# Performance work log

Hardware: AMD Instinct MI355X
Metric: run time of the kernel (lower is better)

The kernel has to match this reference:

```python
import jax, jax.numpy as jnp
import numpy as np
from jax import lax

D_MODEL, D_STATE, D_CONV = 64, 16, 4
D_INNER = 2 * D_MODEL          # expand=2 -> 128
DT_RANK = (D_MODEL + 15) // 16 # 4
DIM_IN, LIN_DIM, DIM_OUT = 5881, 128, 256
B, T = 64, 256


def setup_inputs() -> dict:
    key = jax.random.key(0)
    ks = jax.random.split(key, 20)
    s = 0.02
    inp = {
        "input": jax.random.normal(ks[0], (B, T, DIM_IN), dtype=jnp.float32),
        # encoder (SparseLinear dim_in -> 64)
        "W_enc": jax.random.normal(ks[1], (D_MODEL, DIM_IN), dtype=jnp.float32) * s,
        "b_enc": jax.random.normal(ks[2], (D_MODEL,), dtype=jnp.float32) * s,
        # Mamba params
        "W_in": jax.random.normal(ks[3], (2 * D_INNER, D_MODEL), dtype=jnp.float32) * s,
        "conv_w": jax.random.normal(ks[4], (D_INNER, D_CONV), dtype=jnp.float32) * s,
        "conv_b": jax.random.normal(ks[5], (D_INNER,), dtype=jnp.float32) * s,
        "W_x": jax.random.normal(ks[6], (DT_RANK + 2 * D_STATE, D_INNER), dtype=jnp.float32) * s,
        "W_dt": jax.random.normal(ks[7], (D_INNER, DT_RANK), dtype=jnp.float32) * s,
        "b_dt": jax.random.normal(ks[8], (D_INNER,), dtype=jnp.float32) * s,
        "A_log": jnp.log(jnp.broadcast_to(jnp.arange(1, D_STATE + 1, dtype=jnp.float32), (D_INNER, D_STATE))),
        "D_skip": jnp.ones((D_INNER,), dtype=jnp.float32),
        "W_out": jax.random.normal(ks[9], (D_MODEL, D_INNER), dtype=jnp.float32) * s,
        # heads
        "W_fc": jax.random.normal(ks[10], (LIN_DIM, D_MODEL), dtype=jnp.float32) * s,
        "b_fc": jax.random.normal(ks[11], (LIN_DIM,), dtype=jnp.float32) * s,
        "W_mu": jax.random.normal(ks[12], (DIM_OUT, LIN_DIM), dtype=jnp.float32) * s,
        "b_mu": jax.random.normal(ks[13], (DIM_OUT,), dtype=jnp.float32) * s,
        "W_sig": jax.random.normal(ks[14], (DIM_OUT, LIN_DIM), dtype=jnp.float32) * s,
        "b_sig": jax.random.normal(ks[15], (DIM_OUT,), dtype=jnp.float32) * s,
    }
    return inp


def _mamba(z, W_in, conv_w, conv_b, W_x, W_dt, b_dt, A_log, D_skip, W_out):
    # z: [B, T, d_model]
    xz = jnp.einsum("btm,im->bti", z, W_in)            # [B,T,2*Di]
    x, gate = jnp.split(xz, 2, axis=-1)                 # each [B,T,Di]
    # causal depthwise conv1d, kernel D_CONV
    xp = jnp.pad(x, ((0, 0), (D_CONV - 1, 0), (0, 0)))
    x_conv = sum(xp[:, k:k + x.shape[1], :] * conv_w[:, k] for k in range(D_CONV)) + conv_b
    x_conv = jax.nn.silu(x_conv)
    # input-dependent SSM params
    x_dbl = jnp.einsum("btd,id->bti", x_conv, W_x)      # [B,T,dt_rank+2N]
    dt, Bm, Cm = jnp.split(x_dbl, [DT_RANK, DT_RANK + D_STATE], axis=-1)
    dt = jax.nn.softplus(jnp.einsum("btr,dr->btd", dt, W_dt) + b_dt)  # [B,T,Di]
    A = -jnp.exp(A_log)                                 # [Di,N]
    dA = jnp.exp(dt[..., None] * A)                     # [B,T,Di,N]
    dBx = dt[..., None] * Bm[:, :, None, :] * x_conv[..., None]  # [B,T,Di,N]
    # selective scan over time
    def step(h, inp):
        dA_t, dBx_t, C_t = inp
        h = dA_t * h + dBx_t
        y = jnp.einsum("bdn,bn->bd", h, C_t)
        return h, y
    h0 = jnp.zeros((z.shape[0], D_INNER, D_STATE), dtype=z.dtype)
    _, ys = lax.scan(step, h0, (jnp.moveaxis(dA, 1, 0), jnp.moveaxis(dBx, 1, 0), jnp.moveaxis(Cm, 1, 0)))
    y = jnp.moveaxis(ys, 0, 1) + D_skip * x_conv        # [B,T,Di]
    y = y * jax.nn.silu(gate)
    return jnp.einsum("btd,md->btm", y, W_out)          # [B,T,d_model]


def reference(input, W_enc, b_enc, W_in, conv_w, conv_b, W_x, W_dt, b_dt,
              A_log, D_skip, W_out, W_fc, b_fc, W_mu, b_mu, W_sig, b_sig):
    # per-timestep (sparse) linear encoder, vectorized over time
    z = jnp.einsum("btf,df->btd", input, W_enc) + b_enc   # [B,T,64]
    e = _mamba(z, W_in, conv_w, conv_b, W_x, W_dt, b_dt, A_log, D_skip, W_out)
    e = e.mean(axis=1)                                    # [B,64]; dropout = identity (eval)
    x = jax.nn.elu(jnp.tanh(e @ W_fc.T + b_fc))           # [B,128]
    mu = x @ W_mu.T + b_mu                                # [B,256]
    sigma = jax.nn.elu(x @ W_sig.T + b_sig) + 1.0 + 1e-14 # [B,256]
    return (x, mu, sigma)
```

## Files before the change

### kernel.cpp

```cpp
#include <hip/hip_runtime.h>

typedef unsigned short u16;
typedef unsigned int   u32;

#define BB   64
#define TT   256
#define DIN  5881
#define DM   64
#define DI   128
#define NST  16
#define DTR  4
#define TCH  32
#define NCH  8

#define NROW (BB*TT)
#define NKT  92
#define KHALF 46

#define ZWS_OFF  ((size_t)0)
#define WP_OFF   ((size_t)2*1024*1024)
#define PSG_OFF  ((size_t)3*1024*1024)
#define BC_OFF   ((size_t)35*1024*1024)
#define YS_OFF   ((size_t)37*1024*1024)

__device__ __forceinline__ float bf2f(u16 u) {
    union { u32 i; float f; } v; v.i = ((u32)u) << 16; return v.f;
}
__device__ __forceinline__ u16 f2bf(float f) {
    union { float f; u32 i; } v; v.f = f;
    u32 x = v.i;
    return (u16)((x + 0x7FFFu + ((x >> 16) & 1u)) >> 16);
}

typedef __attribute__((ext_vector_type(8))) short short8;
typedef __attribute__((ext_vector_type(4))) float floatx4;

template<bool BF16>
__device__ __forceinline__ float ld1(const void* p, size_t i) {
    if (BF16) return bf2f(((const u16*)p)[i]);
    else      return ((const float*)p)[i];
}
template<bool BF16>
__device__ __forceinline__ u16 ldb(const void* p, size_t i) {
    if (BF16) return ((const u16*)p)[i];
    else      return f2bf(((const float*)p)[i]);
}
template<bool BF16>
__device__ __forceinline__ void st1(void* p, size_t i, float v) {
    if (BF16) ((u16*)p)[i] = f2bf(v);
    else      ((float*)p)[i] = v;
}

__device__ __forceinline__ short8 as_s8(uint4 v) {
    union { uint4 u; short8 s; } c; c.u = v; return c.s;
}

template<bool BF16>
__device__ __forceinline__ void pack_body(const void* Wenc, u16* wp) {
    int g = blockIdx.x * 256 + threadIdx.x;
    if (g >= NKT * 8 * 64) return;
    int lane = g & 63;  int p = g >> 6;
    int kt = p & 1, nt = (p >> 1) & 3, it = p >> 3;
    int r16 = lane & 15, quad = lane >> 4;
    int n  = nt * 16 + r16;
    int k0 = it * 64 + kt * 32 + quad * 8;
    u32 w[4];
    #pragma unroll
    for (int j = 0; j < 4; ++j) {
        int ka = k0 + 2 * j;
        u32 lo = (ka     < DIN) ? (u32)ldb<BF16>(Wenc, (size_t)n * DIN + ka)     : 0u;
        u32 hi = (ka + 1 < DIN) ? (u32)ldb<BF16>(Wenc, (size_t)n * DIN + ka + 1) : 0u;
        w[j] = lo | (hi << 16);
    }
    *(uint4*)(wp + ((size_t)p * 64 + lane) * 8) = make_uint4(w[0], w[1], w[2], w[3]);
}

__global__ __launch_bounds__(256) void pack_wenc(const void* Wenc, const void* A_log, u16* wp) {
    if (((const u32*)A_log)[0] != 0u) pack_body<true >(Wenc, wp);
    else                              pack_body<false>(Wenc, wp);
}

template<bool BF16>
__device__ __forceinline__ void enc_load(const void* inp, const uint4* wp4,
        size_t arow, int it, int kq, int lane, bool tail,
        uint4 a[2], uint4 b[4][2]) {
    #pragma unroll
    for (int kt = 0; kt < 2; ++kt) {
        int k0 = it * 64 + kt * 32 + kq;
        u32 w[4];
        #pragma unroll
        for (int j = 0; j < 4; ++j) {
            u32 lo, hi;
            if (!tail) {
                lo = ldb<BF16>(inp, arow + k0 + 2 * j);
                hi = ldb<BF16>(inp, arow + k0 + 2 * j + 1);
            } else {
                int ka = k0 + 2 * j;
                lo = (ka     < DIN) ? (u32)ldb<BF16>(inp, arow + ka)     : 0u;
                hi = (ka + 1 < DIN) ? (u32)ldb<BF16>(inp, arow + ka + 1) : 0u;
            }
            w[j] = lo | (hi << 16);
        }
        a[kt] = make_uint4(w[0], w[1], w[2], w[3]);
    }
    const uint4* p = wp4 + (size_t)it * 512 + lane;
    #pragma unroll
    for (int nt = 0; nt < 4; ++nt)
        #pragma unroll
        for (int kt = 0; kt < 2; ++kt)
            b[nt][kt] = p[(nt * 2 + kt) * 64];
}

__device__ __forceinline__ void enc_mma(const uint4 a[2], const uint4 b[4][2], floatx4 acc[4]) {
    #pragma unroll
    for (int nt = 0; nt < 4; ++nt)
        #pragma unroll
        for (int kt = 0; kt < 2; ++kt)
            acc[nt] = __builtin_amdgcn_mfma_f32_16x16x32_bf16(
                          as_s8(a[kt]), as_s8(b[nt][kt]), acc[nt], 0, 0, 0);
}

template<bool BF16>
__device__ __forceinline__ void enc_body(const void* inp, const void* benc,
                                         const u16* wp, u16* z, float* zred) {
    const int tid  = threadIdx.x;
    const int wave = tid >> 6, lane = tid & 63;
    const int r16  = lane & 15, quad = lane >> 4;
    const int half = wave >> 2, mt = wave & 3;
    const int m0   = blockIdx.x * 64 + mt * 16;
    const size_t arow = (size_t)(m0 + r16) * DIN;
    const int kq = quad * 8;
    const uint4* wp4 = (const uint4*)wp;
    const int it0 = half * KHALF, itN = it0 + KHALF;

    floatx4 acc[4];
    #pragma unroll
    for (int nt = 0; nt < 4; ++nt) acc[nt] = (floatx4){0, 0, 0, 0};

    uint4 aA[2], bA[4][2], aB[2], bB[4][2];
    enc_load<BF16>(inp, wp4, arow, it0, kq, lane, false, aA, bA);
    for (int it = it0; it < itN; it += 2) {
        enc_load<BF16>(inp, wp4, arow, it + 1, kq, lane, (it + 1) == NKT - 1, aB, bB);
        enc_mma(aA, bA, acc);
        if (it + 2 < itN)
            enc_load<BF16>(inp, wp4, arow, it + 2, kq, lane, false, aA, bA);
        enc_mma(aB, bB, acc);
    }

    if (half == 0) {
        #pragma unroll
        for (int nt = 0; nt < 4; ++nt)
            #pragma unroll
            for (int reg = 0; reg < 4; ++reg)
                zred[(mt * 16 + quad * 4 + reg) * 64 + nt * 16 + r16] = acc[nt][reg];
    }
    __syncthreads();
    if (half == 1) {
        #pragma unroll
        for (int nt = 0; nt < 4; ++nt) {
            float bi = ld1<BF16>(benc, nt * 16 + r16);
            #pragma unroll
            for (int reg = 0; reg < 4; ++reg) {
                int lr = mt * 16 + quad * 4 + reg;
                float v = zred[lr * 64 + nt * 16 + r16] + acc[nt][reg] + bi;
                z[(size_t)(blockIdx.x * 64 + lr) * DM + nt * 16 + r16] = f2bf(v);
            }
        }
    }
}

__global__ __launch_bounds__(512) void enc_gemm(const void* inp, const void* benc,
                                                const void* A_log, const u16* wp, u16* z) {
    __shared__ __align__(16) float zred[64 * 64];
    if (((const u32*)A_log)[0] != 0u) enc_body<true >(inp, benc, wp, z, zred);
    else                              enc_body<false>(inp, benc, wp, z, zred);
}

template<bool BF16>
__device__ __forceinline__ void prep_body(
        const void* W_in, const void* conv_w, const void* conv_b,
        const void* W_x, const void* W_dt, const void* b_dt, const void* D_skip,
        const u16* zws, float4* psg, float* BCg,
        u16* zc, u16* xl, u16* gl, u16* xcb, float* xd2) {

    const int bid  = blockIdx.x;
    const int b    = bid >> 3, c = bid & 7;
    const int tid  = threadIdx.x;
    const int wave = tid >> 6, lane = tid & 63;
    const int quad = lane >> 4, r16 = lane & 15;
    const int dd   = tid & 127;

    float cw[4], cb, wdt[4], bdt, Dv;
    #pragma unroll
    for (int k = 0; k < 4; ++k) cw[k] = ld1<BF16>(conv_w, dd * 4 + k);
    cb = ld1<BF16>(conv_b, dd);
    #pragma unroll
    for (int r = 0; r < 4; ++r) wdt[r] = ld1<BF16>(W_dt, dd * 4 + r);
    bdt = ld1<BF16>(b_dt, dd);
    Dv  = ld1<BF16>(D_skip, dd);

    short8 win[4][2];
    #pragma unroll
    for (int nt = 0; nt < 4; ++nt)
        #pragma unroll
        for (int kt = 0; kt < 2; ++kt) {
            size_t base = (size_t)(wave * 64 + nt * 16 + r16) * DM + kt * 32 + quad * 8;
            short8 v;
            #pragma unroll
            for (int e = 0; e < 8; ++e) v[e] = (short)ldb<BF16>(W_in, base + e);
            win[nt][kt] = v;
        }

    short8 wx[4];
    {
        int j = wave * 16 + r16;
        #pragma unroll
        for (int kt = 0; kt < 4; ++kt) {
            short8 v = (short8){0,0,0,0,0,0,0,0};
            if (wave < 3 && j < DTR + 2 * NST) {
                size_t base = (size_t)j * DI + kt * 32 + quad * 8;
                #pragma unroll
                for (int e = 0; e < 8; ++e) v[e] = (short)ldb<BF16>(W_x, base + e);
            }
            wx[kt] = v;
        }
    }

    const int base_t = c * 32 - 16;
    for (int i = tid; i < 48 * 64; i += 256) {
        int rr = i >> 6, nn = i & 63, t = base_t + rr;
        u16 v = 0;
        if (t >= 0) v = zws[(size_t)(b * TT + t) * DM + nn];
        zc[rr * 72 + nn] = v;
    }
    __syncthreads();

    floatx4 xza[3][4];
    #pragma unroll
    for (int mt = 0; mt < 3; ++mt)
        #pragma unroll
        for (int nt = 0; nt < 4; ++nt) xza[mt][nt] = (floatx4){0,0,0,0};
    #pragma unroll
    for (int kt = 0; kt < 2; ++kt) {
        short8 a[3];
        #pragma unroll
        for (int mt = 0; mt < 3; ++mt)
            a[mt] = *(const short8*)(&zc[(mt * 16 + r16) * 72 + kt * 32 + quad * 8]);
        #pragma unroll
        for (int nt = 0; nt < 4; ++nt)
            #pragma unroll
            for (int mt = 0; mt < 3; ++mt)
                xza[mt][nt] = __builtin_amdgcn_mfma_f32_16x16x32_bf16(a[mt], win[nt][kt], xza[mt][nt], 0, 0, 0);
    }
    #pragma unroll
    for (int mt = 0; mt < 3; ++mt)
        #pragma unroll
        for (int nt = 0; nt < 4; ++nt) {
            int n = wave * 64 + nt * 16 + r16;
            #pragma unroll
            for (int reg = 0; reg < 4; ++reg) {
                int rr = mt * 16 + quad * 4 + reg;
                u16 v = f2bf(xza[mt][nt][reg]);
                if (n < DI) { if (rr >= 13) xl[(rr - 13) * 128 + n] = v; }
                else if (rr >= 16) gl[(rr - 16) * 128 + (n - DI)] = v;
            }
        }
    __syncthreads();

    for (int it2 = tid; it2 < TCH * DI; it2 += 256) {
        int t = it2 >> 7, d = it2 & 127;
        float a = cb;
        #pragma unroll
        for (int k = 0; k < 4; ++k) a += bf2f(xl[(t + k) * 128 + d]) * cw[k];
        float s = a / (1.f + expf(-a));
        xcb[t * 136 + d] = f2bf(s);
    }
    __syncthreads();

    {
        floatx4 xda0 = (floatx4){0,0,0,0}, xda1 = (floatx4){0,0,0,0};
        if (wave < 3) {
            #pragma unroll
            for (int kt = 0; kt < 4; ++kt) {
                short8 a0 = *(const short8*)(&xcb[(0 * 16 + r16) * 136 + kt * 32 + quad * 8]);
                short8 a1 = *(const short8*)(&xcb[(1 * 16 + r16) * 136 + kt * 32 + quad * 8]);
                xda0 = __builtin_amdgcn_mfma_f32_16x16x32_bf16(a0, wx[kt], xda0, 0, 0, 0);
                xda1 = __builtin_amdgcn_mfma_f32_16x16x32_bf16(a1, wx[kt], xda1, 0, 0, 0);
            }
            int j = wave * 16 + r16;
            if (j < DTR + 2 * NST) {
                #pragma unroll
                for (int reg = 0; reg < 4; ++reg) {
                    xd2[(0 * 16 + quad * 4 + reg) * 40 + j] = xda0[reg];
                    xd2[(1 * 16 + quad * 4 + reg) * 40 + j] = xda1[reg];
                }
            }
        }
    }
    __syncthreads();

    const size_t rowb = (size_t)b * TT + c * 32;
    for (int it2 = tid; it2 < TCH * DI; it2 += 256) {
        int t = it2 >> 7, d = it2 & 127;
        float v = bdt;
        #pragma unroll
        for (int r = 0; r < 4; ++r) v += xd2[t * 40 + r] * wdt[r];
        float sp  = (v > 20.f) ? v : log1pf(expf(v));
        float xcv = bf2f(xcb[t * 136 + d]);
        float g   = bf2f(gl[t * 128 + d]);
        float sg  = g / (1.f + expf(-g));
        psg[(rowb + t) * DI + d] = make_float4(sp, sp * xcv, sg, Dv * xcv * sg);
    }
    for (int i = tid; i < TCH * 32; i += 256) {
        int t = i >> 5, j = i & 31;
        BCg[(rowb + t) * 32 + j] = xd2[t * 40 + DTR + j];
    }
}

__global__ __launch_bounds__(256) void prep(
        const void* W_in, const void* conv_w, const void* conv_b,
        const void* W_x, const void* W_dt, const void* b_dt, const void* D_skip,
        const void* A_log, const u16* zws, float4* psg, float* BCg) {
    __shared__ __align__(16) u16  zc[48 * 72];
    __shared__ __align__(16) u16  xl[35 * 128];
    __shared__ __align__(16) u16  gl[32 * 128];
    __shared__ __align__(16) u16  xcb[32 * 136];
    __shared__ __align__(16) float xd2[32 * 40];
    if (((const u32*)A_log)[0] != 0u)
        prep_body<true >(W_in, conv_w, conv_b, W_x, W_dt, b_dt, D_skip, zws, psg, BCg,
                         zc, xl, gl, xcb, xd2);
    else
        prep_body<false>(W_in, conv_w, conv_b, W_x, W_dt, b_dt, D_skip, zws, psg, BCg,
                         zc, xl, gl, xcb, xd2);
}

__device__ __forceinline__ void scan_ld(const float4* psg, const float* BCg,
        size_t pbase, size_t bbase, int s, float4 (&P)[8], float (&Bv)[8], float (&Cv)[8]) {
    #pragma unroll
    for (int q = 0; q < 8; ++q) {
        int r = s * 8 + q;
        P[q]  = psg[pbase + (size_t)r * DI];
        Bv[q] = BCg[bbase + (size_t)r * 32];
        Cv[q] = BCg[bbase + (size_t)r * 32 + 16];
    }
}
__device__ __forceinline__ void scan_cmp(const float4 (&P)[8], const float (&Bv)[8],
        const float (&Cv)[8], float Av, int n, float& h, float& acc, float& sk) {
    #pragma unroll
    for (int q = 0; q < 8; ++q) {
        float e = expf(P[q].x * Av);
        h   = fmaf(e, h, P[q].y * Bv[q]);
        acc = fmaf(h * Cv[q], P[q].z, acc);
        sk += (n == 0) ? P[q].w : 0.f;
    }
}

__global__ __launch_bounds__(512) void scan_k(const void* A_log, const float4* psg,
        const float* BCg, float* ysg) {
    const int tid = threadIdx.x;
    const int b = blockIdx.x >> 2, dq = blockIdx.x & 3;
    const int dl = tid >> 4, n = tid & 15;
    const int d = dq * 32 + dl;
    const bool isbf = (((const u32*)A_log)[0] != 0u);
    float al = isbf ? bf2f(((const u16*)A_log)[d * NST + n])
                    : ((const float*)A_log)[d * NST + n];
    const float Av = -expf(al);
    const size_t rb = (size_t)b * TT;
    const size_t pbase = rb * DI + d;
    const size_t bbase = rb * 32 + n;

    float4 pA[8], pB[8];
    float  BA[8], CA[8], Bb[8], Cb[8];
    float h = 0.f, acc = 0.f, sk = 0.f;

    scan_ld(psg, BCg, pbase, bbase, 0, pA, BA, CA);
    for (int s = 0; s < 32; s += 2) {
        scan_ld(psg, BCg, pbase, bbase, s + 1, pB, Bb, Cb);
        scan_cmp(pA, BA, CA, Av, n, h, acc, sk);
        if (s + 2 < 32) scan_ld(psg, BCg, pbase, bbase, s + 2, pA, BA, CA);
        scan_cmp(pB, Bb, Cb, Av, n, h, acc, sk);
    }
    acc += __shfl_xor(acc, 1);
    acc += __shfl_xor(acc, 2);
    acc += __shfl_xor(acc, 4);
    acc += __shfl_xor(acc, 8);
    if (n == 0) ysg[(size_t)b * DI + d] = acc + sk;
}

template<bool BF16>
__device__ __forceinline__ void heads_body(
        const void* W_out, const void* W_fc, const void* b_fc,
        const void* W_mu, const void* b_mu, const void* W_sig, const void* b_sig,
        const float* ysg, void* out, float* yb, float* es, float* xs) {
    const int b = blockIdx.x, tid = threadIdx.x;
    if (tid < DI) yb[tid] = ysg[(size_t)b * DI + tid] * (1.f / (float)TT);
    __syncthreads();
    if (tid < DM) {
        float s = 0.f;
        #pragma unroll 8
        for (int k = 0; k < DI; ++k) s += yb[k] * ld1<BF16>(W_out, (size_t)tid * DI + k);
        es[tid] = s;
    }
    __syncthreads();
    if (tid < 128) {
        float s = ld1<BF16>(b_fc, tid);
        #pragma unroll 8
        for (int k = 0; k < DM; ++k) s += es[k] * ld1<BF16>(W_fc, (size_t)tid * DM + k);
        float th = tanhf(s);
        float xv = th > 0.f ? th : expm1f(th);
        xs[tid] = xv;
        st1<BF16>(out, (size_t)b * 128 + tid, xv);
    }
    __syncthreads();
    for (int j = tid; j < 512; j += 256) {
        int o = j & 255;
        bool is_mu = (j < 256);
        const void* w = is_mu ? W_mu : W_sig;
        float s = ld1<BF16>(is_mu ? b_mu : b_sig, o);
        #pragma unroll 8
        for (int k = 0; k < 128; ++k) s += xs[k] * ld1<BF16>(w, (size_t)o * 128 + k);
        if (is_mu) {
            st1<BF16>(out, 8192 + (size_t)b * 256 + o, s);
        } else {
            float e = s > 0.f ? s : expm1f(s);
            st1<BF16>(out, 8192 + 16384 + (size_t)b * 256 + o, e + 1.f + 1e-14f);
        }
    }
}

__global__ __launch_bounds__(256) void heads_k(
        const void* W_out, const void* W_fc, const void* b_fc,
        const void* W_mu, const void* b_mu, const void* W_sig, const void* b_sig,
        const void* A_log, const float* ysg, void* out) {
    __shared__ float yb[128];
    __shared__ float es[64];
    __shared__ float xs[128];
    if (((const u32*)A_log)[0] != 0u)
        heads_body<true >(W_out, W_fc, b_fc, W_mu, b_mu, W_sig, b_sig, ysg, out, yb, es, xs);
    else
        heads_body<false>(W_out, W_fc, b_fc, W_mu, b_mu, W_sig, b_sig, ysg, out, yb, es, xs);
}

extern "C" void kernel_launch(void* const* d_in, const int* in_sizes, int n_in,
                              void* d_out, int out_size, void* d_ws, size_t ws_size,
                              hipStream_t stream) {
    (void)in_sizes; (void)n_in; (void)ws_size; (void)out_size;
    char* ws = (char*)d_ws;
    u16*    zws = (u16*)(ws + ZWS_OFF);
    u16*    wp  = (u16*)(ws + WP_OFF);
    float4* psg = (float4*)(ws + PSG_OFF);
    float*  BCg = (float*)(ws + BC_OFF);
    float*  ysg = (float*)(ws + YS_OFF);

    pack_wenc<<<184, 256, 0, stream>>>(d_in[1], d_in[9], wp);
    enc_gemm<<<256, 512, 0, stream>>>(d_in[0], d_in[2], d_in[9], wp, zws);
    prep<<<512, 256, 0, stream>>>(d_in[3], d_in[4], d_in[5], d_in[6], d_in[7],
                                  d_in[8], d_in[10], d_in[9], zws, psg, BCg);
    scan_k<<<256, 512, 0, stream>>>(d_in[9], psg, BCg, ysg);
    heads_k<<<64, 256, 0, stream>>>(d_in[11], d_in[12], d_in[13], d_in[14],
                                    d_in[15], d_in[16], d_in[17], d_in[9], ysg, d_out);
}
```

Baseline: 717.2 us.

## Restructure encoder GEMM for coalesced row loads via LDS staging and split-K

The encoder GEMM now assigns 16 rows per block and splits K across four waves. Each lane loads one column element across 16 rows, so the loads coalesce along K. The data is staged through per-wave LDS to form the MFMA A fragments, replacing the previous strided per-lane 8-element gathers along each row. The grid grows to 1024 blocks of 256 threads, and a four-way LDS reduction sums the partial results. This targets the memory efficiency of streaming the large input, at the cost of extra LDS traffic and the reduction step.

```diff
diff --git a/kernel.cpp b/kernel.cpp
--- a/kernel.cpp
+++ b/kernel.cpp
@@ -15,7 +15,7 @@
 
 #define NROW (BB*TT)
 #define NKT  92
-#define KHALF 46
+#define KQRT 23
 
 #define ZWS_OFF  ((size_t)0)
 #define WP_OFF   ((size_t)2*1024*1024)
@@ -81,99 +81,102 @@
 }
 
 template<bool BF16>
-__device__ __forceinline__ void enc_load(const void* inp, const uint4* wp4,
-        size_t arow, int it, int kq, int lane, bool tail,
-        uint4 a[2], uint4 b[4][2]) {
-    #pragma unroll
-    for (int kt = 0; kt < 2; ++kt) {
-        int k0 = it * 64 + kt * 32 + kq;
-        u32 w[4];
-        #pragma unroll
-        for (int j = 0; j < 4; ++j) {
-            u32 lo, hi;
-            if (!tail) {
-                lo = ldb<BF16>(inp, arow + k0 + 2 * j);
-                hi = ldb<BF16>(inp, arow + k0 + 2 * j + 1);
-            } else {
-                int ka = k0 + 2 * j;
-                lo = (ka     < DIN) ? (u32)ldb<BF16>(inp, arow + ka)     : 0u;
-                hi = (ka + 1 < DIN) ? (u32)ldb<BF16>(inp, arow + ka + 1) : 0u;
-            }
-            w[j] = lo | (hi << 16);
-        }
-        a[kt] = make_uint4(w[0], w[1], w[2], w[3]);
-    }
+__device__ __forceinline__ void enc_loadr(const void* inp, int m0, int it, int lane,
+                                          u16 (&rg)[16]) {
+    const size_t kb = (size_t)it * 64 + lane;
+    if (it != NKT - 1) {
+        #pragma unroll
+        for (int j = 0; j < 16; ++j)
+            rg[j] = ldb<BF16>(inp, (size_t)(m0 + j) * DIN + kb);
+    } else {
+        bool ok = kb < DIN;
+        #pragma unroll
+        for (int j = 0; j < 16; ++j)
+            rg[j] = ok ? ldb<BF16>(inp, (size_t)(m0 + j) * DIN + kb) : (u16)0;
+    }
+}
+
+__device__ __forceinline__ void enc_write(u16* ms, int lane, const u16 (&rg)[16]) {
+    #pragma unroll
+    for (int j = 0; j < 16; ++j) ms[j * 72 + lane] = rg[j];
+}
+
+__device__ __forceinline__ void enc_compute(int it, const uint4* wp4, int lane,
+                                            int r16, int quad, const u16* ms,
+                                            floatx4 (&acc)[4]) {
+    uint4 b[4][2];
     const uint4* p = wp4 + (size_t)it * 512 + lane;
     #pragma unroll
     for (int nt = 0; nt < 4; ++nt)
         #pragma unroll
         for (int kt = 0; kt < 2; ++kt)
             b[nt][kt] = p[(nt * 2 + kt) * 64];
-}
-
-__device__ __forceinline__ void enc_mma(const uint4 a[2], const uint4 b[4][2], floatx4 acc[4]) {
-    #pragma unroll
-    for (int nt = 0; nt < 4; ++nt)
-        #pragma unroll
-        for (int kt = 0; kt < 2; ++kt)
-            acc[nt] = __builtin_amdgcn_mfma_f32_16x16x32_bf16(
-                          as_s8(a[kt]), as_s8(b[nt][kt]), acc[nt], 0, 0, 0);
+    short8 a0 = *(const short8*)(ms + r16 * 72 +  0 + quad * 8);
+    short8 a1 = *(const short8*)(ms + r16 * 72 + 32 + quad * 8);
+    #pragma unroll
+    for (int nt = 0; nt < 4; ++nt) {
+        acc[nt] = __builtin_amdgcn_mfma_f32_16x16x32_bf16(a0, as_s8(b[nt][0]), acc[nt], 0, 0, 0);
+        acc[nt] = __builtin_amdgcn_mfma_f32_16x16x32_bf16(a1, as_s8(b[nt][1]), acc[nt], 0, 0, 0);
+    }
 }
 
 template<bool BF16>
 __device__ __forceinline__ void enc_body(const void* inp, const void* benc,
-                                         const u16* wp, u16* z, float* zred) {
+                                         const u16* wp, u16* z,
+                                         u16* stg, float* zred) {
     const int tid  = threadIdx.x;
     const int wave = tid >> 6, lane = tid & 63;
     const int r16  = lane & 15, quad = lane >> 4;
-    const int half = wave >> 2, mt = wave & 3;
-    const int m0   = blockIdx.x * 64 + mt * 16;
-    const size_t arow = (size_t)(m0 + r16) * DIN;
-    const int kq = quad * 8;
+    const int m0   = blockIdx.x * 16;
     const uint4* wp4 = (const uint4*)wp;
-    const int it0 = half * KHALF, itN = it0 + KHALF;
+    u16* ms = stg + wave * (16 * 72);
+    const int it0 = wave * KQRT;
 
     floatx4 acc[4];
     #pragma unroll
     for (int nt = 0; nt < 4; ++nt) acc[nt] = (floatx4){0, 0, 0, 0};
 
-    uint4 aA[2], bA[4][2], aB[2], bB[4][2];
-    enc_load<BF16>(inp, wp4, arow, it0, kq, lane, false, aA, bA);
-    for (int it = it0; it < itN; it += 2) {
-        enc_load<BF16>(inp, wp4, arow, it + 1, kq, lane, (it + 1) == NKT - 1, aB, bB);
-        enc_mma(aA, bA, acc);
-        if (it + 2 < itN)
-            enc_load<BF16>(inp, wp4, arow, it + 2, kq, lane, false, aA, bA);
-        enc_mma(aB, bB, acc);
-    }
-
-    if (half == 0) {
-        #pragma unroll
-        for (int nt = 0; nt < 4; ++nt)
-            #pragma unroll
-            for (int reg = 0; reg < 4; ++reg)
-                zred[(mt * 16 + quad * 4 + reg) * 64 + nt * 16 + r16] = acc[nt][reg];
-    }
-    __syncthreads();
-    if (half == 1) {
-        #pragma unroll
-        for (int nt = 0; nt < 4; ++nt) {
-            float bi = ld1<BF16>(benc, nt * 16 + r16);
-            #pragma unroll
-            for (int reg = 0; reg < 4; ++reg) {
-                int lr = mt * 16 + quad * 4 + reg;
-                float v = zred[lr * 64 + nt * 16 + r16] + acc[nt][reg] + bi;
-                z[(size_t)(blockIdx.x * 64 + lr) * DM + nt * 16 + r16] = f2bf(v);
-            }
-        }
-    }
-}
-
-__global__ __launch_bounds__(512) void enc_gemm(const void* inp, const void* benc,
+    u16 rgA[16], rgB[16];
+    enc_loadr<BF16>(inp, m0, it0, lane, rgA);
+    int it = it0;
+    #pragma unroll 1
+    for (int p = 0; p < (KQRT - 1) / 2; ++p, it += 2) {
+        enc_write(ms, lane, rgA);
+        enc_loadr<BF16>(inp, m0, it + 1, lane, rgB);
+        enc_compute(it, wp4, lane, r16, quad, ms, acc);
+        enc_write(ms, lane, rgB);
+        enc_loadr<BF16>(inp, m0, it + 2, lane, rgA);
+        enc_compute(it + 1, wp4, lane, r16, quad, ms, acc);
+    }
+    enc_write(ms, lane, rgA);
+    enc_compute(it, wp4, lane, r16, quad, ms, acc);
+
+    #pragma unroll
+    for (int nt = 0; nt < 4; ++nt) {
+        int col = nt * 16 + r16;
+        #pragma unroll
+        for (int reg = 0; reg < 4; ++reg) {
+            int row = quad * 4 + reg;
+            zred[wave * 1024 + row * 64 + col] = acc[nt][reg];
+        }
+    }
+    __syncthreads();
+    #pragma unroll
+    for (int rep = 0; rep < 4; ++rep) {
+        int o = rep * 256 + tid;
+        int col = o & 63;
+        float s = zred[o] + zred[1024 + o] + zred[2048 + o] + zred[3072 + o]
+                + ld1<BF16>(benc, col);
+        z[(size_t)(m0 + (o >> 6)) * DM + col] = f2bf(s);
+    }
+}
+
+__global__ __launch_bounds__(256) void enc_gemm(const void* inp, const void* benc,
                                                 const void* A_log, const u16* wp, u16* z) {
-    __shared__ __align__(16) float zred[64 * 64];
-    if (((const u32*)A_log)[0] != 0u) enc_body<true >(inp, benc, wp, z, zred);
-    else                              enc_body<false>(inp, benc, wp, z, zred);
+    __shared__ __align__(16) u16   stg[4 * 16 * 72];
+    __shared__ __align__(16) float zred[4 * 1024];
+    if (((const u32*)A_log)[0] != 0u) enc_body<true >(inp, benc, wp, z, stg, zred);
+    else                              enc_body<false>(inp, benc, wp, z, stg, zred);
 }
 
 template<bool BF16>
@@ -453,7 +456,7 @@
     float*  ysg = (float*)(ws + YS_OFF);
 
     pack_wenc<<<184, 256, 0, stream>>>(d_in[1], d_in[9], wp);
-    enc_gemm<<<256, 512, 0, stream>>>(d_in[0], d_in[2], d_in[9], wp, zws);
+    enc_gemm<<<1024, 256, 0, stream>>>(d_in[0], d_in[2], d_in[9], wp, zws);
     prep<<<512, 256, 0, stream>>>(d_in[3], d_in[4], d_in[5], d_in[6], d_in[7],
                                   d_in[8], d_in[10], d_in[9], zws, psg, BCg);
     scan_k<<<256, 512, 0, stream>>>(d_in[9], psg, BCg, ysg);
```

Result: faster. 642.3 us (-10.4%).
